# Kernel tuning notes

Hardware: AMD Instinct MI355X
Metric: run time of the kernel (lower is better)

## Reference

```python
import jax, jax.numpy as jnp
import numpy as np

B, NB, BD, H = 524288, 8, 16, 64  # batch, n_bundles, bundle_dim, hidden_dim

def setup_inputs() -> dict:
    key = jax.random.key(0)
    ks = jax.random.split(key, 8)
    z = jax.random.normal(ks[0], (B, NB, BD), dtype=jnp.float32)
    w1 = jax.random.normal(ks[1], (H, NB), dtype=jnp.float32) * (1.0 / np.sqrt(NB))
    b1 = jnp.zeros((H,), dtype=jnp.float32)
    w2 = jax.random.normal(ks[2], (H, H), dtype=jnp.float32) * (1.0 / np.sqrt(H))
    b2 = jnp.zeros((H,), dtype=jnp.float32)
    w3 = jax.random.normal(ks[3], (NB, H), dtype=jnp.float32) * (1.0 / np.sqrt(H))
    mix_w = jax.random.normal(ks[4], (NB, NB, BD, BD), dtype=jnp.float32) * 0.01
    gate_bias = jnp.zeros((NB,), dtype=jnp.float32)
    return {"z": z, "w1": w1, "b1": b1, "w2": w2, "b2": b2, "w3": w3,
            "mix_w": mix_w, "gate_bias": gate_bias}

def reference(z, w1, b1, w2, b2, w3, mix_w, gate_bias):
    # per-bundle norms: [B, NB]
    norms = jnp.linalg.norm(z, axis=-1) + 1e-8
    # tiny gating MLP (exact GELU like torch nn.GELU default)
    h = jax.nn.gelu(norms @ w1.T + b1, approximate=False)
    h = jax.nn.gelu(h @ w2.T + b2, approximate=False)
    scales = jax.nn.softplus(h @ w3.T)                      # [B, NB]
    equivariant = z * scales[:, :, None]                    # [B, NB, BD]
    # cross-bundle mixing: mixing[b,i,k] = sum_{j,d} z[b,j,d] * W[i,j,k,d]
    mixing = jnp.einsum('bjd,ijkd->bik', z, mix_w)          # [B, NB, BD]
    gates = jax.nn.sigmoid(gate_bias)[None, :, None]        # [1, NB, 1]
    return z + (equivariant + gates * mixing)
```

## Files before the change

kernel.cpp:

```cpp
#include <hip/hip_runtime.h>
#include <hip/hip_fp16.h>

typedef __bf16 bf16x8 __attribute__((ext_vector_type(8)));
typedef float  f32x4  __attribute__((ext_vector_type(4)));
typedef _Float16 half2v __attribute__((ext_vector_type(2)));
typedef unsigned short ushort8 __attribute__((ext_vector_type(8)));

__device__ __forceinline__ unsigned short f2bf(float f){
  unsigned u = __builtin_bit_cast(unsigned, f);
  u = (u + 0x7FFFu + ((u >> 16) & 1u)) >> 16;
  return (unsigned short)u;
}

#if defined(__has_builtin)
#  if __has_builtin(__builtin_amdgcn_fdot2)
#    define FDOT2(a,b,c) __builtin_amdgcn_fdot2((a),(b),(c),false)
#  endif
#endif
#ifndef FDOT2
__device__ __forceinline__ float fdot2_sw(half2v a, half2v b, float c){
  return c + (float)a[0]*(float)b[0] + (float)a[1]*(float)b[1];
}
#  define FDOT2(a,b,c) fdot2_sw((a),(b),(c))
#endif

__device__ __forceinline__ float gelu_fast(float x){
  float u = 0.7978845608f * x * __builtin_fmaf(0.044715f, x * x, 1.0f);
  float e = __expf(2.0f * __builtin_fabsf(u));
  float t = 1.0f - 2.0f / (e + 1.0f);
  t = __builtin_copysignf(t, u);
  return 0.5f * x * (1.0f + t);
}

__device__ __forceinline__ float softplus_fast(float x){
  float e = __expf(-__builtin_fabsf(x));
  return fmaxf(x, 0.0f) + __logf(1.0f + e);
}

__global__ void prepack_wt(const float* __restrict__ mix_w,
                           unsigned short* __restrict__ wt){
  int tid = blockIdx.x * 256 + threadIdx.x;
  int f = tid >> 6, L = tid & 63;
  int ks = f & 3, nt = f >> 2;
  int q = L >> 4, c = L & 15;
  int N = nt * 16 + c;
  int i = N >> 4, ko = N & 15;
  unsigned pk[4];
#pragma unroll
  for (int p = 0; p < 4; ++p){
    int K0 = ks * 32 + q * 8 + 2 * p;
    int K1 = K0 + 1;
    unsigned lo = f2bf(mix_w[((i*8 + (K0>>4))*16 + ko)*16 + (K0&15)]);
    unsigned hi = f2bf(mix_w[((i*8 + (K1>>4))*16 + ko)*16 + (K1&15)]);
    pk[p] = lo | (hi << 16);
  }
  uint4 v; v.x = pk[0]; v.y = pk[1]; v.z = pk[2]; v.w = pk[3];
  ((uint4*)wt)[tid] = v;
}

__global__ __launch_bounds__(256, 3)
void soft_eq_kernel(const float* __restrict__ z,
                    const float* __restrict__ w1,  const float* __restrict__ b1,
                    const float* __restrict__ w2,  const float* __restrict__ b2,
                    const float* __restrict__ w3,  const float* __restrict__ gate_bias,
                    const unsigned short* __restrict__ wt,
                    float* __restrict__ out){
  __shared__ float    zsm[64][132];
  __shared__ float    normsS[64][8];
  __shared__ _Float16 h1s[64][64];
  __shared__ _Float16 h2s[64][64];
  __shared__ float    gatesS[8];
  float (*scalesS)[8] = (float(*)[8])h1s;

  const int t = threadIdx.x;
  const size_t base = (size_t)blockIdx.x * (64 * 128);
  const float4* zg = (const float4*)(z + base);

#pragma unroll
  for (int it = 0; it < 8; ++it){
    int idx = t + it * 256;
    float4 v = zg[idx];
    int r  = idx >> 5;
    int c4 = (idx & 31) * 4;
    *(float4*)&zsm[r][c4] = v;
    float ss = v.x*v.x + v.y*v.y + v.z*v.z + v.w*v.w;
    ss += __shfl_xor(ss, 1);
    ss += __shfl_xor(ss, 2);
    if ((t & 3) == 0) normsS[r][c4 >> 4] = sqrtf(ss) + 1e-8f;
  }

  const int i = t & 63;
  float w1r[8];
  { const float4* p = (const float4*)(w1 + i * 8);
    float4 a = p[0], bq = p[1];
    w1r[0]=a.x; w1r[1]=a.y; w1r[2]=a.z; w1r[3]=a.w;
    w1r[4]=bq.x; w1r[5]=bq.y; w1r[6]=bq.z; w1r[7]=bq.w; }
  const float b1r = b1[i], b2r = b2[i];
  half2v wreg[32];
  { const float4* p = (const float4*)(w2 + i * 64);
#pragma unroll
    for (int kk = 0; kk < 16; ++kk){
      float4 v = p[kk];
      wreg[2*kk]   = half2v{(_Float16)v.x, (_Float16)v.y};
      wreg[2*kk+1] = half2v{(_Float16)v.z, (_Float16)v.w};
    } }
  if (t < 8) gatesS[t] = 1.0f / (1.0f + __expf(-gate_bias[t]));

  __syncthreads();

  const int rg = t >> 6;
#pragma unroll
  for (int chunk = 0; chunk < 16; ++chunk){
    int r = chunk * 4 + rg;
    const float4* np = (const float4*)&normsS[r][0];
    float4 n0 = np[0], n1 = np[1];
    float pre = b1r + n0.x*w1r[0] + n0.y*w1r[1] + n0.z*w1r[2] + n0.w*w1r[3]
                    + n1.x*w1r[4] + n1.y*w1r[5] + n1.z*w1r[6] + n1.w*w1r[7];
    h1s[r][i] = (_Float16)gelu_fast(pre);
  }
  __syncthreads();

#pragma unroll
  for (int chunk = 0; chunk < 16; ++chunk){
    int r = chunk * 4 + rg;
    const uint4* hp = (const uint4*)&h1s[r][0];
    float a0 = b2r, a1 = 0.f, a2 = 0.f, a3 = 0.f;
#pragma unroll
    for (int kk = 0; kk < 8; ++kk){
      uint4 hv = hp[kk];
      a0 = FDOT2(__builtin_bit_cast(half2v, hv.x), wreg[4*kk+0], a0);
      a1 = FDOT2(__builtin_bit_cast(half2v, hv.y), wreg[4*kk+1], a1);
      a2 = FDOT2(__builtin_bit_cast(half2v, hv.z), wreg[4*kk+2], a2);
      a3 = FDOT2(__builtin_bit_cast(half2v, hv.w), wreg[4*kk+3], a3);
    }
    float accv = (a0 + a1) + (a2 + a3);
    h2s[r][i] = (_Float16)gelu_fast(accv);
  }

  { const float4* p = (const float4*)(w3 + (t & 7) * 64);
#pragma unroll
    for (int kk = 0; kk < 16; ++kk){
      float4 v = p[kk];
      wreg[2*kk]   = half2v{(_Float16)v.x, (_Float16)v.y};
      wreg[2*kk+1] = half2v{(_Float16)v.z, (_Float16)v.w};
    } }
  __syncthreads();

#pragma unroll
  for (int s = 0; s < 2; ++s){
    int item = s * 256 + t;
    int r = item >> 3, j = item & 7;
    const uint4* hp = (const uint4*)&h2s[r][0];
    float a0 = 0.f, a1 = 0.f, a2 = 0.f, a3 = 0.f;
#pragma unroll
    for (int kk = 0; kk < 8; ++kk){
      uint4 hv = hp[kk];
      a0 = FDOT2(__builtin_bit_cast(half2v, hv.x), wreg[4*kk+0], a0);
      a1 = FDOT2(__builtin_bit_cast(half2v, hv.y), wreg[4*kk+1], a1);
      a2 = FDOT2(__builtin_bit_cast(half2v, hv.z), wreg[4*kk+2], a2);
      a3 = FDOT2(__builtin_bit_cast(half2v, hv.w), wreg[4*kk+3], a3);
    }
    scalesS[r][j] = softplus_fast((a0 + a1) + (a2 + a3));
  }
  __syncthreads();

  const int w = t >> 6, L = t & 63, q = L >> 4, c = L & 15;
  f32x4 acc[8] = {};
  const uint4* wtf = (const uint4*)wt;
  const int am = w * 16 + c;
#pragma unroll
  for (int ks = 0; ks < 4; ++ks){
    int ak = ks * 32 + q * 8;
    float4 a0 = *(const float4*)&zsm[am][ak];
    float4 a1 = *(const float4*)&zsm[am][ak + 4];
    ushort8 au;
    au[0]=f2bf(a0.x); au[1]=f2bf(a0.y); au[2]=f2bf(a0.z); au[3]=f2bf(a0.w);
    au[4]=f2bf(a1.x); au[5]=f2bf(a1.y); au[6]=f2bf(a1.z); au[7]=f2bf(a1.w);
    bf16x8 af = __builtin_bit_cast(bf16x8, au);
#pragma unroll
    for (int n = 0; n < 8; ++n){
      uint4 bv = wtf[(n * 4 + ks) * 64 + L];
      bf16x8 bfr = __builtin_bit_cast(bf16x8, bv);
      acc[n] = __builtin_amdgcn_mfma_f32_16x16x32_bf16(af, bfr, acc[n], 0, 0, 0);
    }
  }

  float* op = out + base;
#pragma unroll
  for (int n = 0; n < 8; ++n){
    float gate = gatesS[n];
#pragma unroll
    for (int rr = 0; rr < 4; ++rr){
      int row = w * 16 + q * 4 + rr;
      int col = n * 16 + c;
      float zv = zsm[row][col];
      float sc = scalesS[row][n];
      op[row * 128 + col] = zv + zv * sc + gate * acc[n][rr];
    }
  }
}

extern "C" void kernel_launch(void* const* d_in, const int* in_sizes, int n_in,
                              void* d_out, int out_size, void* d_ws, size_t ws_size,
                              hipStream_t stream){
  const float* z         = (const float*)d_in[0];
  const float* w1        = (const float*)d_in[1];
  const float* b1        = (const float*)d_in[2];
  const float* w2        = (const float*)d_in[3];
  const float* b2        = (const float*)d_in[4];
  const float* w3        = (const float*)d_in[5];
  const float* mix_w     = (const float*)d_in[6];
  const float* gate_bias = (const float*)d_in[7];
  float* out = (float*)d_out;
  unsigned short* wt = (unsigned short*)d_ws;

  int B = in_sizes[0] / 128;
  prepack_wt<<<8, 256, 0, stream>>>(mix_w, wt);
  soft_eq_kernel<<<B / 64, 256, 0, stream>>>(z, w1, b1, w2, b2, w3, gate_bias, wt, out);
}
```

Baseline: 609.1 us.

## Move gating MLP layers to f16 MFMA and drop z shared-memory staging

Replaces the fdot2-based hidden and output MLP layers with 16x16x32 f16 MFMA instructions, using XOR-swizzled shared-memory layouts for h1/h2. It removes the 33KB z tile from LDS and re-reads z from global memory (expected to hit L2/cache) for the mixing matmul and epilogue, which raises the occupancy target from 3 to 5 blocks per CU. It also uses rcp-based GELU and fused FMAs in the epilogue. The tradeoff is extra global reads of z, and w2/w3 are now loaded and converted per wave from global memory instead of held in registers.

```diff
diff --git a/kernel.cpp b/kernel.cpp
--- a/kernel.cpp
+++ b/kernel.cpp
@@ -1,9 +1,9 @@
 #include <hip/hip_runtime.h>
 #include <hip/hip_fp16.h>
 
-typedef __bf16 bf16x8 __attribute__((ext_vector_type(8)));
-typedef float  f32x4  __attribute__((ext_vector_type(4)));
-typedef _Float16 half2v __attribute__((ext_vector_type(2)));
+typedef __bf16   bf16x8 __attribute__((ext_vector_type(8)));
+typedef _Float16 f16x8  __attribute__((ext_vector_type(8)));
+typedef float    f32x4  __attribute__((ext_vector_type(4)));
 typedef unsigned short ushort8 __attribute__((ext_vector_type(8)));
 
 __device__ __forceinline__ unsigned short f2bf(float f){
@@ -12,22 +12,10 @@
   return (unsigned short)u;
 }
 
-#if defined(__has_builtin)
-#  if __has_builtin(__builtin_amdgcn_fdot2)
-#    define FDOT2(a,b,c) __builtin_amdgcn_fdot2((a),(b),(c),false)
-#  endif
-#endif
-#ifndef FDOT2
-__device__ __forceinline__ float fdot2_sw(half2v a, half2v b, float c){
-  return c + (float)a[0]*(float)b[0] + (float)a[1]*(float)b[1];
-}
-#  define FDOT2(a,b,c) fdot2_sw((a),(b),(c))
-#endif
-
 __device__ __forceinline__ float gelu_fast(float x){
   float u = 0.7978845608f * x * __builtin_fmaf(0.044715f, x * x, 1.0f);
   float e = __expf(2.0f * __builtin_fabsf(u));
-  float t = 1.0f - 2.0f / (e + 1.0f);
+  float t = __builtin_fmaf(-2.0f, __builtin_amdgcn_rcpf(e + 1.0f), 1.0f);
   t = __builtin_copysignf(t, u);
   return 0.5f * x * (1.0f + t);
 }
@@ -58,19 +46,18 @@
   ((uint4*)wt)[tid] = v;
 }
 
-__global__ __launch_bounds__(256, 3)
+__global__ __launch_bounds__(256, 5)
 void soft_eq_kernel(const float* __restrict__ z,
                     const float* __restrict__ w1,  const float* __restrict__ b1,
                     const float* __restrict__ w2,  const float* __restrict__ b2,
                     const float* __restrict__ w3,  const float* __restrict__ gate_bias,
                     const unsigned short* __restrict__ wt,
                     float* __restrict__ out){
-  __shared__ float    zsm[64][132];
-  __shared__ float    normsS[64][8];
-  __shared__ _Float16 h1s[64][64];
-  __shared__ _Float16 h2s[64][64];
-  __shared__ float    gatesS[8];
-  float (*scalesS)[8] = (float(*)[8])h1s;
+  __shared__ __align__(16) _Float16 h1s[64 * 64];
+  __shared__ __align__(16) _Float16 h2s[64 * 64];
+  __shared__ float gatesS[8];
+  float (*normsS)[8] = (float(*)[8])h2s;
+  float (*scalesS)[9] = (float(*)[9])h1s;
 
   const int t = threadIdx.x;
   const size_t base = (size_t)blockIdx.x * (64 * 128);
@@ -81,98 +68,103 @@
     int idx = t + it * 256;
     float4 v = zg[idx];
     int r  = idx >> 5;
-    int c4 = (idx & 31) * 4;
-    *(float4*)&zsm[r][c4] = v;
+    int bi = (idx & 31) >> 2;
     float ss = v.x*v.x + v.y*v.y + v.z*v.z + v.w*v.w;
     ss += __shfl_xor(ss, 1);
     ss += __shfl_xor(ss, 2);
-    if ((t & 3) == 0) normsS[r][c4 >> 4] = sqrtf(ss) + 1e-8f;
-  }
-
-  const int i = t & 63;
+    if ((t & 3) == 0) normsS[r][bi] = sqrtf(ss) + 1e-8f;
+  }
+
+  const int i = t & 63, rg = t >> 6;
   float w1r[8];
   { const float4* p = (const float4*)(w1 + i * 8);
     float4 a = p[0], bq = p[1];
     w1r[0]=a.x; w1r[1]=a.y; w1r[2]=a.z; w1r[3]=a.w;
     w1r[4]=bq.x; w1r[5]=bq.y; w1r[6]=bq.z; w1r[7]=bq.w; }
-  const float b1r = b1[i], b2r = b2[i];
-  half2v wreg[32];
-  { const float4* p = (const float4*)(w2 + i * 64);
-#pragma unroll
-    for (int kk = 0; kk < 16; ++kk){
-      float4 v = p[kk];
-      wreg[2*kk]   = half2v{(_Float16)v.x, (_Float16)v.y};
-      wreg[2*kk+1] = half2v{(_Float16)v.z, (_Float16)v.w};
-    } }
-  if (t < 8) gatesS[t] = 1.0f / (1.0f + __expf(-gate_bias[t]));
-
-  __syncthreads();
-
-  const int rg = t >> 6;
+  const float b1r = b1[i];
+  __syncthreads();
+
 #pragma unroll
   for (int chunk = 0; chunk < 16; ++chunk){
     int r = chunk * 4 + rg;
-    const float4* np = (const float4*)&normsS[r][0];
+    const float4* np = (const float4*)normsS[r];
     float4 n0 = np[0], n1 = np[1];
     float pre = b1r + n0.x*w1r[0] + n0.y*w1r[1] + n0.z*w1r[2] + n0.w*w1r[3]
                     + n1.x*w1r[4] + n1.y*w1r[5] + n1.z*w1r[6] + n1.w*w1r[7];
-    h1s[r][i] = (_Float16)gelu_fast(pre);
-  }
-  __syncthreads();
-
-#pragma unroll
-  for (int chunk = 0; chunk < 16; ++chunk){
-    int r = chunk * 4 + rg;
-    const uint4* hp = (const uint4*)&h1s[r][0];
-    float a0 = b2r, a1 = 0.f, a2 = 0.f, a3 = 0.f;
-#pragma unroll
-    for (int kk = 0; kk < 8; ++kk){
-      uint4 hv = hp[kk];
-      a0 = FDOT2(__builtin_bit_cast(half2v, hv.x), wreg[4*kk+0], a0);
-      a1 = FDOT2(__builtin_bit_cast(half2v, hv.y), wreg[4*kk+1], a1);
-      a2 = FDOT2(__builtin_bit_cast(half2v, hv.z), wreg[4*kk+2], a2);
-      a3 = FDOT2(__builtin_bit_cast(half2v, hv.w), wreg[4*kk+3], a3);
-    }
-    float accv = (a0 + a1) + (a2 + a3);
-    h2s[r][i] = (_Float16)gelu_fast(accv);
-  }
-
-  { const float4* p = (const float4*)(w3 + (t & 7) * 64);
-#pragma unroll
-    for (int kk = 0; kk < 16; ++kk){
-      float4 v = p[kk];
-      wreg[2*kk]   = half2v{(_Float16)v.x, (_Float16)v.y};
-      wreg[2*kk+1] = half2v{(_Float16)v.z, (_Float16)v.w};
-    } }
-  __syncthreads();
-
-#pragma unroll
-  for (int s = 0; s < 2; ++s){
-    int item = s * 256 + t;
-    int r = item >> 3, j = item & 7;
-    const uint4* hp = (const uint4*)&h2s[r][0];
-    float a0 = 0.f, a1 = 0.f, a2 = 0.f, a3 = 0.f;
-#pragma unroll
-    for (int kk = 0; kk < 8; ++kk){
-      uint4 hv = hp[kk];
-      a0 = FDOT2(__builtin_bit_cast(half2v, hv.x), wreg[4*kk+0], a0);
-      a1 = FDOT2(__builtin_bit_cast(half2v, hv.y), wreg[4*kk+1], a1);
-      a2 = FDOT2(__builtin_bit_cast(half2v, hv.z), wreg[4*kk+2], a2);
-      a3 = FDOT2(__builtin_bit_cast(half2v, hv.w), wreg[4*kk+3], a3);
-    }
-    scalesS[r][j] = softplus_fast((a0 + a1) + (a2 + a3));
-  }
-  __syncthreads();
-
-  const int w = t >> 6, L = t & 63, q = L >> 4, c = L & 15;
+    int u = (i >> 3) ^ (r & 7);
+    h1s[r * 64 + u * 8 + (i & 7)] = (_Float16)gelu_fast(pre);
+  }
+  __syncthreads();
+
+  const int w = rg, L = t & 63, q = L >> 4, c = L & 15;
+  const int am = w * 16 + c;
+
+  f16x8 a2[2];
+#pragma unroll
+  for (int ks = 0; ks < 2; ++ks){
+    int u = (ks * 4 + q) ^ (am & 7);
+    a2[ks] = *(const f16x8*)&h1s[am * 64 + u * 8];
+  }
+#pragma unroll
+  for (int nt = 0; nt < 4; ++nt){
+    int n = nt * 16 + c;
+    f32x4 acc2 = {};
+#pragma unroll
+    for (int ks = 0; ks < 2; ++ks){
+      const float4* wp = (const float4*)(w2 + n * 64 + ks * 32 + q * 8);
+      float4 v0 = wp[0], v1 = wp[1];
+      f16x8 bf;
+      bf[0]=(_Float16)v0.x; bf[1]=(_Float16)v0.y; bf[2]=(_Float16)v0.z; bf[3]=(_Float16)v0.w;
+      bf[4]=(_Float16)v1.x; bf[5]=(_Float16)v1.y; bf[6]=(_Float16)v1.z; bf[7]=(_Float16)v1.w;
+      acc2 = __builtin_amdgcn_mfma_f32_16x16x32_f16(a2[ks], bf, acc2, 0, 0, 0);
+    }
+    float b2v = b2[n];
+#pragma unroll
+    for (int rr = 0; rr < 4; ++rr){
+      int row = w * 16 + q * 4 + rr;
+      int uu = (n >> 3) ^ (row & 7);
+      h2s[row * 64 + uu * 8 + (n & 7)] = (_Float16)gelu_fast(acc2[rr] + b2v);
+    }
+  }
+  __syncthreads();
+
+  {
+    f16x8 a3[2];
+#pragma unroll
+    for (int ks = 0; ks < 2; ++ks){
+      int u = (ks * 4 + q) ^ (am & 7);
+      a3[ks] = *(const f16x8*)&h2s[am * 64 + u * 8];
+    }
+    int n3 = c & 7;
+    f32x4 acc3 = {};
+#pragma unroll
+    for (int ks = 0; ks < 2; ++ks){
+      const float4* wp = (const float4*)(w3 + n3 * 64 + ks * 32 + q * 8);
+      float4 v0 = wp[0], v1 = wp[1];
+      f16x8 bf;
+      bf[0]=(_Float16)v0.x; bf[1]=(_Float16)v0.y; bf[2]=(_Float16)v0.z; bf[3]=(_Float16)v0.w;
+      bf[4]=(_Float16)v1.x; bf[5]=(_Float16)v1.y; bf[6]=(_Float16)v1.z; bf[7]=(_Float16)v1.w;
+      acc3 = __builtin_amdgcn_mfma_f32_16x16x32_f16(a3[ks], bf, acc3, 0, 0, 0);
+    }
+    if (c < 8){
+#pragma unroll
+      for (int rr = 0; rr < 4; ++rr){
+        int row = w * 16 + q * 4 + rr;
+        scalesS[row][c] = softplus_fast(acc3[rr]);
+      }
+    }
+  }
+  if (t < 8) gatesS[t] = __builtin_amdgcn_rcpf(1.0f + __expf(-gate_bias[t]));
+  __syncthreads();
+
   f32x4 acc[8] = {};
   const uint4* wtf = (const uint4*)wt;
-  const int am = w * 16 + c;
+  const float* zp = z + base;
 #pragma unroll
   for (int ks = 0; ks < 4; ++ks){
     int ak = ks * 32 + q * 8;
-    float4 a0 = *(const float4*)&zsm[am][ak];
-    float4 a1 = *(const float4*)&zsm[am][ak + 4];
+    const float4* ap = (const float4*)(zp + am * 128 + ak);
+    float4 a0 = ap[0], a1 = ap[1];
     ushort8 au;
     au[0]=f2bf(a0.x); au[1]=f2bf(a0.y); au[2]=f2bf(a0.z); au[3]=f2bf(a0.w);
     au[4]=f2bf(a1.x); au[5]=f2bf(a1.y); au[6]=f2bf(a1.z); au[7]=f2bf(a1.w);
@@ -193,9 +185,9 @@
     for (int rr = 0; rr < 4; ++rr){
       int row = w * 16 + q * 4 + rr;
       int col = n * 16 + c;
-      float zv = zsm[row][col];
+      float zv = zp[row * 128 + col];
       float sc = scalesS[row][n];
-      op[row * 128 + col] = zv + zv * sc + gate * acc[n][rr];
+      op[row * 128 + col] = __builtin_fmaf(zv, sc, __builtin_fmaf(gate, acc[n][rr], zv));
     }
   }
 }
```

Result: faster. 575.7 us (-5.5%).
